# Optimization experiments

Measured on AMD Instinct MI355X. Metric: run time of the kernel, lower is better.

Reference implementation:

```python
import jax, jax.numpy as jnp
import numpy as np

D_MODEL = 256
N_HEADS = 8
HEAD_DIM = D_MODEL // N_HEADS  # 32
N_LEVELS = 4
N_POINTS = 4
LEVEL_SHAPES = [(100, 100), (50, 50), (25, 25), (13, 13)]
LEVEL_STARTS = [0] + list(np.cumsum([h * w for h, w in LEVEL_SHAPES]))[:-1]
LEN_IN = int(sum(h * w for h, w in LEVEL_SHAPES))  # 13294
BATCH = 2
LEN_Q = LEN_IN  # encoder self-attention


def _offset_bias():
    # faithful to MSDeformAttn._reset_parameters for sampling_offsets bias
    thetas = np.arange(N_HEADS, dtype=np.float32) * (2.0 * np.pi / N_HEADS)
    grid = np.stack([np.cos(thetas), np.sin(thetas)], -1)
    grid = grid / np.abs(grid).max(-1, keepdims=True)
    grid = np.tile(grid.reshape(N_HEADS, 1, 1, 2), (1, N_LEVELS, N_POINTS, 1))
    for i in range(N_POINTS):
        grid[:, :, i, :] *= i + 1
    return jnp.asarray(grid.reshape(-1), dtype=jnp.float32)


def setup_inputs() -> dict:
    key = jax.random.key(0)
    ks = jax.random.split(key, 10)
    s = 1.0 / np.sqrt(D_MODEL)
    inp = {
        "query": jax.random.normal(ks[0], (BATCH, LEN_Q, D_MODEL), jnp.float32),
        "reference_points": jax.random.uniform(ks[1], (BATCH, LEN_Q, N_LEVELS, 2), jnp.float32),
        "input_flatten": jax.random.normal(ks[2], (BATCH, LEN_IN, D_MODEL), jnp.float32),
        "input_spatial_shapes": jnp.asarray(LEVEL_SHAPES, dtype=jnp.int32),
        "W_value": jax.random.normal(ks[3], (D_MODEL, D_MODEL), jnp.float32) * s,
        "b_value": jnp.zeros((D_MODEL,), jnp.float32),
        "W_off": jax.random.normal(ks[4], (D_MODEL, N_HEADS * N_LEVELS * N_POINTS * 2), jnp.float32) * 0.01,
        "b_off": _offset_bias(),
        "W_attn": jax.random.normal(ks[5], (D_MODEL, N_HEADS * N_LEVELS * N_POINTS), jnp.float32) * 0.01,
        "b_attn": jnp.zeros((N_HEADS * N_LEVELS * N_POINTS,), jnp.float32),
        "W_out": jax.random.normal(ks[6], (D_MODEL, D_MODEL), jnp.float32) * s,
        "b_out": jnp.zeros((D_MODEL,), jnp.float32),
    }
    return inp


def _corner(v_t, ix, iy, h, w):
    # v_t: (n, M, h*w, D); ix/iy: (n, M, LqP) int32. Zero padding outside.
    valid = (ix >= 0) & (ix < w) & (iy >= 0) & (iy < h)
    idx = jnp.clip(iy, 0, h - 1) * w + jnp.clip(ix, 0, w - 1)
    g = jnp.take_along_axis(v_t, idx[..., None], axis=2)  # (n, M, LqP, D)
    return g * valid[..., None].astype(v_t.dtype)


def _ms_deform_attn(query, reference_points, input_flatten,
                    W_value, b_value, W_off, b_off, W_attn, b_attn, W_out, b_out):
    n, lq, _ = query.shape
    value = (input_flatten @ W_value + b_value).reshape(n, LEN_IN, N_HEADS, HEAD_DIM)
    offs = (query @ W_off + b_off).reshape(n, lq, N_HEADS, N_LEVELS, N_POINTS, 2)
    aw = jax.nn.softmax(
        (query @ W_attn + b_attn).reshape(n, lq, N_HEADS, N_LEVELS * N_POINTS), axis=-1
    ).reshape(n, lq, N_HEADS, N_LEVELS, N_POINTS)
    # offset_normalizer = (w, h) per level
    norm = jnp.asarray([[w, h] for h, w in LEVEL_SHAPES], dtype=query.dtype)
    loc = reference_points[:, :, None, :, None, :] + offs / norm[None, None, None, :, None, :]

    acc = jnp.zeros((n, N_HEADS, lq, HEAD_DIM), dtype=value.dtype)
    for l, (h, w) in enumerate(LEVEL_SHAPES):
        s0 = LEVEL_STARTS[l]
        v_t = jnp.transpose(value[:, s0:s0 + h * w], (0, 2, 1, 3))  # (n, M, hw, D)
        ll = loc[:, :, :, l]  # (n, lq, M, P, 2) in [0,1]
        # grid_sample bilinear, align_corners=False: pixel = coord*size - 0.5
        x = ll[..., 0] * w - 0.5
        y = ll[..., 1] * h - 0.5
        x0 = jnp.floor(x); y0 = jnp.floor(y)
        tx = x - x0; ty = y - y0
        ix0 = x0.astype(jnp.int32); iy0 = y0.astype(jnp.int32)
        flat = lambda a: jnp.transpose(a, (0, 2, 1, 3)).reshape(n, N_HEADS, lq * N_POINTS)
        ix0f, iy0f = flat(ix0), flat(iy0)
        txf = flat(tx)[..., None]; tyf = flat(ty)[..., None]
        g00 = _corner(v_t, ix0f, iy0f, h, w)
        g01 = _corner(v_t, ix0f + 1, iy0f, h, w)
        g10 = _corner(v_t, ix0f, iy0f + 1, h, w)
        g11 = _corner(v_t, ix0f + 1, iy0f + 1, h, w)
        samp = (g00 * (1 - txf) * (1 - tyf) + g01 * txf * (1 - tyf)
                + g10 * (1 - txf) * tyf + g11 * txf * tyf)
        samp = samp.reshape(n, N_HEADS, lq, N_POINTS, HEAD_DIM)
        wl = jnp.transpose(aw[:, :, :, l], (0, 2, 1, 3))[..., None]  # (n, M, lq, P, 1)
        acc = acc + (samp * wl).sum(axis=3)

    out = jnp.transpose(acc, (0, 2, 1, 3)).reshape(n, lq, D_MODEL)
    return out @ W_out + b_out


def reference(query, reference_points, input_flatten, input_spatial_shapes,
              W_value, b_value, W_off, b_off, W_attn, b_attn, W_out, b_out):
    # input_spatial_shapes carried for signature fidelity; level geometry is static.
    return _ms_deform_attn(query, reference_points, input_flatten,
                           W_value, b_value, W_off, b_off, W_attn, b_attn, W_out, b_out)
```

## Files before the change

### kernel.cpp

```cpp
#include <hip/hip_runtime.h>

#define NH 8
#define HD 32
#define NL 4
#define NP 4
#define DM 256
#define LEN_IN_C 13294
#define LQ_C 13294
#define B_C 2
#define M_TOTAL (B_C * LQ_C)
#define MT_TILES 1662
#define MT_PAD 1664
#define RBLK (MT_PAD / 4)

typedef __attribute__((ext_vector_type(8))) short short8;
typedef __attribute__((ext_vector_type(4))) float floatx4;

__device__ __forceinline__ unsigned short f2bf(float x) {
    union { float f; unsigned int u; } a; a.f = x;
    unsigned int r = (a.u + 0x7FFFu + ((a.u >> 16) & 1u)) >> 16;
    return (unsigned short)r;
}
__device__ __forceinline__ float bflo(unsigned int u) {
    union { unsigned int u; float f; } a; a.u = u << 16; return a.f;
}
__device__ __forceinline__ float bfhi(unsigned int u) {
    union { unsigned int u; float f; } a; a.u = u & 0xffff0000u; return a.f;
}

__device__ __forceinline__ void glds16(const void* g, void* l) {
    __builtin_amdgcn_global_load_lds(
        (const __attribute__((address_space(1))) unsigned int*)g,
        (__attribute__((address_space(3))) unsigned int*)l, 16, 0, 0);
}

__global__ __launch_bounds__(256) void conv_a_kernel(const float* __restrict__ A0,
                                                     unsigned short* __restrict__ D0,
                                                     const float* __restrict__ A1,
                                                     unsigned short* __restrict__ D1,
                                                     int M) {
    const float* A = blockIdx.y ? A1 : A0;
    unsigned short* Asw = blockIdx.y ? D1 : D0;
    const int u = blockIdx.x * 256 + threadIdx.x;
    const int lane = u & 63;
    const int kc = (u >> 6) & 7;
    const int rt = u >> 9;
    const int row = rt * 16 + (lane & 15);
    const int col0 = kc * 32 + (lane >> 4) * 8;
    unsigned short tmp[8];
    if (row < M) {
        const float4 f0 = *(const float4*)(A + (size_t)row * 256 + col0);
        const float4 f1 = *(const float4*)(A + (size_t)row * 256 + col0 + 4);
        tmp[0] = f2bf(f0.x); tmp[1] = f2bf(f0.y); tmp[2] = f2bf(f0.z); tmp[3] = f2bf(f0.w);
        tmp[4] = f2bf(f1.x); tmp[5] = f2bf(f1.y); tmp[6] = f2bf(f1.z); tmp[7] = f2bf(f1.w);
    } else {
#pragma unroll
        for (int j = 0; j < 8; ++j) tmp[j] = 0;
    }
    short8 v;
#pragma unroll
    for (int j = 0; j < 8; ++j) v[j] = (short)tmp[j];
    ((short8*)Asw)[u] = v;
}

__device__ __forceinline__ void conv_b_body(const float* __restrict__ W,
                                            unsigned short* __restrict__ Bsw,
                                            int Nsrc, int NTsrc, int NTtotal, int ntOff,
                                            int vblk) {
    const int u = vblk * 256 + threadIdx.x;
    const int lane = u & 63;
    const int unit = u >> 6;
    const int ntl = unit % NTsrc;
    const int kc = unit / NTsrc;
    const int n = ntl * 16 + (lane & 15);
    const int k0 = kc * 32 + (lane >> 4) * 8;
    short8 v;
#pragma unroll
    for (int j = 0; j < 8; ++j)
        v[j] = (short)f2bf(W[(size_t)(k0 + j) * Nsrc + n]);
    ((short8*)Bsw)[(size_t)(kc * NTtotal + ntOff + ntl) * 64 + lane] = v;
}

__global__ __launch_bounds__(256) void conv_weights_kernel(const float* __restrict__ Wv,
                                                           const float* __restrict__ Woff,
                                                           const float* __restrict__ Wattn,
                                                           const float* __restrict__ Wout,
                                                           const float* __restrict__ boff,
                                                           const float* __restrict__ battn,
                                                           unsigned short* __restrict__ BswV,
                                                           unsigned short* __restrict__ BswOA,
                                                           unsigned short* __restrict__ BswO,
                                                           float* __restrict__ fbias) {
    const int blk = blockIdx.x;
    if (blk < 32)        conv_b_body(Wv,    BswV,  256, 16, 16, 0,  blk);
    else if (blk < 64)   conv_b_body(Woff,  BswOA, 256, 16, 24, 0,  blk - 32);
    else if (blk < 80)   conv_b_body(Wattn, BswOA, 128,  8, 24, 16, blk - 64);
    else if (blk < 112)  conv_b_body(Wout,  BswO,  256, 16, 16, 0,  blk - 80);
    else {
        const int t = (blk - 112) * 256 + threadIdx.x;
        if (t < 384) fbias[t] = (t < 256) ? boff[t] : battn[t - 256];
    }
}

template <bool OUT_BF16, int NT_B, int NCOLS>
__device__ __forceinline__ void gemm_lds_body(short8* As, short8* Bs,
                                              const short8* __restrict__ Au,
                                              const short8* __restrict__ Bu,
                                              int rtile0, int ntB,
                                              const float* __restrict__ bias,
                                              void* __restrict__ Cout, int M) {
    const int tid = threadIdx.x;
    const int lane = tid & 63;
    const int wave = tid >> 6;

#pragma unroll
    for (int i = 0; i < 8; ++i)
        glds16(&Au[(size_t)((rtile0 + wave) * 8 + i) * 64 + lane], &As[(wave * 8 + i) * 64]);
#pragma unroll
    for (int j = 0; j < 2; ++j) {
        const int u = wave * 2 + j;
        glds16(&Bu[(size_t)(ntB + u) * 64 + lane], &Bs[u * 64]);
    }
    __syncthreads();

    floatx4 acc[4][2];
#pragma unroll
    for (int r = 0; r < 4; ++r)
#pragma unroll
        for (int j = 0; j < 2; ++j) acc[r][j] = (floatx4){0.f, 0.f, 0.f, 0.f};

#pragma unroll
    for (int kc = 0; kc < 8; ++kc) {
        if (kc < 7) {
#pragma unroll
            for (int j = 0; j < 2; ++j) {
                const int u = wave * 2 + j;
                glds16(&Bu[(size_t)((kc + 1) * NT_B + ntB + u) * 64 + lane],
                       &Bs[(((kc + 1) & 1) * 8 + u) * 64]);
            }
        }
        const short8 a0 = As[(0 * 8 + kc) * 64 + lane];
        const short8 a1 = As[(1 * 8 + kc) * 64 + lane];
        const short8 a2 = As[(2 * 8 + kc) * 64 + lane];
        const short8 a3 = As[(3 * 8 + kc) * 64 + lane];
        const short8 b0 = Bs[((kc & 1) * 8 + wave * 2 + 0) * 64 + lane];
        const short8 b1 = Bs[((kc & 1) * 8 + wave * 2 + 1) * 64 + lane];
        acc[0][0] = __builtin_amdgcn_mfma_f32_16x16x32_bf16(a0, b0, acc[0][0], 0, 0, 0);
        acc[0][1] = __builtin_amdgcn_mfma_f32_16x16x32_bf16(a0, b1, acc[0][1], 0, 0, 0);
        acc[1][0] = __builtin_amdgcn_mfma_f32_16x16x32_bf16(a1, b0, acc[1][0], 0, 0, 0);
        acc[1][1] = __builtin_amdgcn_mfma_f32_16x16x32_bf16(a1, b1, acc[1][1], 0, 0, 0);
        acc[2][0] = __builtin_amdgcn_mfma_f32_16x16x32_bf16(a2, b0, acc[2][0], 0, 0, 0);
        acc[2][1] = __builtin_amdgcn_mfma_f32_16x16x32_bf16(a2, b1, acc[2][1], 0, 0, 0);
        acc[3][0] = __builtin_amdgcn_mfma_f32_16x16x32_bf16(a3, b0, acc[3][0], 0, 0, 0);
        acc[3][1] = __builtin_amdgcn_mfma_f32_16x16x32_bf16(a3, b1, acc[3][1], 0, 0, 0);
        __syncthreads();
    }

    const int colq = lane & 15;
    const int rowq = (lane >> 4) * 4;
#pragma unroll
    for (int j = 0; j < 2; ++j) {
        const int col = (ntB + wave * 2 + j) * 16 + colq;
        const float bc = bias[col];
#pragma unroll
        for (int r = 0; r < 4; ++r) {
#pragma unroll
            for (int reg = 0; reg < 4; ++reg) {
                const int row = (rtile0 + r) * 16 + rowq + reg;
                if (row < M) {
                    const float v = acc[r][j][reg] + bc;
                    if (OUT_BF16)
                        ((unsigned short*)Cout)[(size_t)row * NCOLS + col] = f2bf(v);
                    else
                        ((float*)Cout)[(size_t)row * NCOLS + col] = v;
                }
            }
        }
    }
}

__global__ __launch_bounds__(256, 3) void dual_gemm_kernel(const short8* __restrict__ AuV,
                                                           const short8* __restrict__ AuQ,
                                                           const short8* __restrict__ BuV,
                                                           const short8* __restrict__ BuOA,
                                                           const float* __restrict__ bv,
                                                           const float* __restrict__ fbias,
                                                           unsigned short* __restrict__ value,
                                                           float* __restrict__ fused, int M) {
    __shared__ short8 As[32 * 64];
    __shared__ short8 Bs[16 * 64];
    const int rtile0 = blockIdx.x * 4;
    const int y = blockIdx.y;
    if (y < 2)
        gemm_lds_body<true, 16, 256>(As, Bs, AuV, BuV, rtile0, y * 8, bv, value, M);
    else
        gemm_lds_body<false, 24, 384>(As, Bs, AuQ, BuOA, rtile0, (y - 2) * 8, fbias, fused, M);
}

__global__ __launch_bounds__(256, 3) void out_gemm_kernel(const short8* __restrict__ AuAcc,
                                                          const short8* __restrict__ BuO,
                                                          const float* __restrict__ bout,
                                                          float* __restrict__ out, int M) {
    __shared__ short8 As[32 * 64];
    __shared__ short8 Bs[16 * 64];
    gemm_lds_body<false, 16, 256>(As, Bs, AuAcc, BuO, blockIdx.x * 4, blockIdx.y * 8,
                                  bout, out, M);
}

__global__ __launch_bounds__(256, 4) void msda_sample_kernel(const float* __restrict__ refp,
                                                             const unsigned short* __restrict__ value,
                                                             const float* __restrict__ fused,
                                                             unsigned short* __restrict__ AccSw) {
    constexpr int lvl_hw[4] = {100, 50, 25, 13};
    constexpr int lvl_s[4] = {0, 10000, 12500, 13125};

    const int bq0 = blockIdx.x * 4;
    const int tid = threadIdx.x;

    __shared__ float s_ref[32];
    __shared__ int4 s_pi[4 * 8 * 17];
    __shared__ float4 s_pw[4 * 8 * 17];

    if (tid < 32) s_ref[tid] = refp[(size_t)bq0 * 8 + tid];
    __syncthreads();

#pragma unroll
    for (int jj = 0; jj < 2; ++jj) {
        const int job = jj * 256 + tid;
        const int qq = job >> 7;
        const int t = job & 127;
        const int h = t >> 4;
        const int l = (t >> 2) & 3;
        const int bq = bq0 + qq;
        const int b = (bq >= LQ_C) ? 1 : 0;

        const float logit = fused[(size_t)bq * 384 + 256 + t];
        float mx = logit;
#pragma unroll
        for (int mask = 1; mask < 16; mask <<= 1) mx = fmaxf(mx, __shfl_xor(mx, mask));
        const float e = expf(logit - mx);
        float s = e;
#pragma unroll
        for (int mask = 1; mask < 16; mask <<= 1) s += __shfl_xor(s, mask);
        const float aw = e / s;

        const int whl = lvl_hw[l];
        const float fwh = (float)whl;
        const float2 oxy = *(const float2*)(fused + (size_t)bq * 384 + t * 2);
        const float x = s_ref[qq * 8 + l * 2] * fwh + oxy.x - 0.5f;
        const float y = s_ref[qq * 8 + l * 2 + 1] * fwh + oxy.y - 0.5f;
        const float x0f = floorf(x), y0f = floorf(y);
        const float tx = x - x0f, ty = y - y0f;
        const int ix0 = (int)x0f, iy0 = (int)y0f;

        const bool xv0 = (unsigned)ix0 < (unsigned)whl;
        const bool xv1 = (unsigned)(ix0 + 1) < (unsigned)whl;
        const bool yv0 = (unsigned)iy0 < (unsigned)whl;
        const bool yv1 = (unsigned)(iy0 + 1) < (unsigned)whl;

        const int cx0 = min(max(ix0, 0), whl - 1);
        const int cx1 = min(max(ix0 + 1, 0), whl - 1);
        const int cy0 = min(max(iy0, 0), whl - 1);
        const int cy1 = min(max(iy0 + 1, 0), whl - 1);

        const int base = (b * LEN_IN_C + lvl_s[l]) * 256 + h * 32;
        const int r0 = base + cy0 * (whl * 256);
        const int r1 = base + cy1 * (whl * 256);
        int4 ii;
        ii.x = (r0 + cx0 * 256) * 2;
        ii.y = (r0 + cx1 * 256) * 2;
        ii.z = (r1 + cx0 * 256) * 2;
        ii.w = (r1 + cx1 * 256) * 2;
        float4 wv;
        wv.x = (xv0 && yv0) ? aw * (1.f - tx) * (1.f - ty) : 0.f;
        wv.y = (xv1 && yv0) ? aw * tx * (1.f - ty) : 0.f;
        wv.z = (xv0 && yv1) ? aw * (1.f - tx) * ty : 0.f;
        wv.w = (xv1 && yv1) ? aw * tx * ty : 0.f;
        const int slot = (qq * 8 + h) * 17 + (t & 15);
        s_pi[slot] = ii;
        s_pw[slot] = wv;
    }
    __syncthreads();

    const int qq = tid >> 6;
    const int h = (tid >> 3) & 7;
    const int l8 = tid & 7;
    const char* vbp = (const char*)value + l8 * 8;
    const int pbase = (qq * 8 + h) * 17;

    float4 acc0 = {0.f, 0.f, 0.f, 0.f};
    float4 acc1 = {0.f, 0.f, 0.f, 0.f};
#pragma unroll
    for (int g = 0; g < 4; ++g) {
        int4 ii[4]; float4 ww[4]; uint2 v[16];
#pragma unroll
        for (int p = 0; p < 4; ++p) {
            ii[p] = s_pi[pbase + g * 4 + p];
            ww[p] = s_pw[pbase + g * 4 + p];
        }
#pragma unroll
        for (int p = 0; p < 4; ++p) {
            v[p * 4 + 0] = *(const uint2*)(vbp + ii[p].x);
            v[p * 4 + 1] = *(const uint2*)(vbp + ii[p].y);
            v[p * 4 + 2] = *(const uint2*)(vbp + ii[p].z);
            v[p * 4 + 3] = *(const uint2*)(vbp + ii[p].w);
        }
#pragma unroll
        for (int p = 0; p < 4; ++p) {
            const float4 wv = ww[p];
            const uint2 v00 = v[p * 4 + 0], v01 = v[p * 4 + 1];
            const uint2 v10 = v[p * 4 + 2], v11 = v[p * 4 + 3];
            acc0.x += wv.x * bflo(v00.x); acc0.y += wv.x * bfhi(v00.x);
            acc0.z += wv.x * bflo(v00.y); acc0.w += wv.x * bfhi(v00.y);
            acc1.x += wv.y * bflo(v01.x); acc1.y += wv.y * bfhi(v01.x);
            acc1.z += wv.y * bflo(v01.y); acc1.w += wv.y * bfhi(v01.y);
            acc0.x += wv.z * bflo(v10.x); acc0.y += wv.z * bfhi(v10.x);
            acc0.z += wv.z * bflo(v10.y); acc0.w += wv.z * bfhi(v10.y);
            acc1.x += wv.w * bflo(v11.x); acc1.y += wv.w * bfhi(v11.x);
            acc1.z += wv.w * bflo(v11.y); acc1.w += wv.w * bfhi(v11.y);
        }
    }
    const float4 acc = {acc0.x + acc1.x, acc0.y + acc1.y, acc0.z + acc1.z, acc0.w + acc1.w};

    const int bq = bq0 + qq;
    const int rt = bq >> 4, mm = bq & 15;
    const int col = h * 32 + l8 * 4;
    const int kc = col >> 5, q2 = (col >> 3) & 3, j = col & 7;
    unsigned int p0 = (unsigned int)f2bf(acc.x) | ((unsigned int)f2bf(acc.y) << 16);
    unsigned int p1 = (unsigned int)f2bf(acc.z) | ((unsigned int)f2bf(acc.w) << 16);
    uint2 pk; pk.x = p0; pk.y = p1;
    *(uint2*)(AccSw + ((size_t)((rt * 8 + kc) * 64 + (q2 * 16 + mm)) * 8 + j)) = pk;
}

extern "C" void kernel_launch(void* const* d_in, const int* in_sizes, int n_in,
                              void* d_out, int out_size, void* d_ws, size_t ws_size,
                              hipStream_t stream) {
    const float* query  = (const float*)d_in[0];
    const float* refp   = (const float*)d_in[1];
    const float* inflat = (const float*)d_in[2];
    const float* Wv    = (const float*)d_in[4];
    const float* bv    = (const float*)d_in[5];
    const float* Woff  = (const float*)d_in[6];
    const float* boff  = (const float*)d_in[7];
    const float* Wattn = (const float*)d_in[8];
    const float* battn = (const float*)d_in[9];
    const float* Wout  = (const float*)d_in[10];
    const float* bout  = (const float*)d_in[11];
    float* out = (float*)d_out;

    char* p = (char*)d_ws;
    const size_t aswBytes = (size_t)MT_PAD * 8 * 64 * 8 * sizeof(unsigned short);
    unsigned short* AswV = (unsigned short*)p;           p += aswBytes;
    unsigned short* AswQ = (unsigned short*)p;           p += aswBytes;
    unsigned short* BswV = (unsigned short*)p;           p += (size_t)8 * 16 * 64 * 8 * 2;
    unsigned short* BswOA = (unsigned short*)p;          p += (size_t)8 * 24 * 64 * 8 * 2;
    unsigned short* BswO = (unsigned short*)p;           p += (size_t)8 * 16 * 64 * 8 * 2;
    float* fbias = (float*)p;                            p += 384 * sizeof(float);
    unsigned short* value = (unsigned short*)p;          p += (size_t)M_TOTAL * 256 * 2;
    float* fused = (float*)p;                            p += (size_t)M_TOTAL * 384 * 4;
    unsigned short* AccSw = AswV;

    const int M = M_TOTAL;

    conv_weights_kernel<<<114, 256, 0, stream>>>(Wv, Woff, Wattn, Wout, boff, battn,
                                                 BswV, BswOA, BswO, fbias);
    conv_a_kernel<<<dim3(MT_PAD * 2, 2), 256, 0, stream>>>(inflat, AswV, query, AswQ, M);
    dual_gemm_kernel<<<dim3(RBLK, 5), 256, 0, stream>>>((const short8*)AswV, (const short8*)AswQ,
                                                        (const short8*)BswV, (const short8*)BswOA,
                                                        bv, fbias, value, fused, M);
    msda_sample_kernel<<<M / 4, 256, 0, stream>>>(refp, value, fused, AccSw);
    out_gemm_kernel<<<dim3(RBLK, 2), 256, 0, stream>>>((const short8*)AccSw, (const short8*)BswO,
                                                       bout, out, M);
}
```

Baseline: 231.1 us.

## Head-major value layout, row-pair sampling, 64-col GEMM tiles, merged conversion kernels

Merges the weight and activation bf16 conversion kernels into one launch. The GEMMs now use 64-column tiles with all of B preloaded into LDS, which removes the per-k syncthreads and double buffering, and the grid is reordered so column blocks vary fastest. The value projection is written head-major so each sampling row segment is contiguous. The sampler therefore loads two 16-byte row pairs per point, with x-clamped edge weights, instead of four 8-byte corners, then reduces across half-lanes with a shuffle. This trades more blocks and a lower occupancy bound for fewer, wider gathers and fewer barriers.

Result: slower. 298.4 us (+29.1%).

```diff
diff --git a/kernel.cpp b/kernel.cpp
--- a/kernel.cpp
+++ b/kernel.cpp
@@ -34,35 +34,6 @@
         (__attribute__((address_space(3))) unsigned int*)l, 16, 0, 0);
 }
 
-__global__ __launch_bounds__(256) void conv_a_kernel(const float* __restrict__ A0,
-                                                     unsigned short* __restrict__ D0,
-                                                     const float* __restrict__ A1,
-                                                     unsigned short* __restrict__ D1,
-                                                     int M) {
-    const float* A = blockIdx.y ? A1 : A0;
-    unsigned short* Asw = blockIdx.y ? D1 : D0;
-    const int u = blockIdx.x * 256 + threadIdx.x;
-    const int lane = u & 63;
-    const int kc = (u >> 6) & 7;
-    const int rt = u >> 9;
-    const int row = rt * 16 + (lane & 15);
-    const int col0 = kc * 32 + (lane >> 4) * 8;
-    unsigned short tmp[8];
-    if (row < M) {
-        const float4 f0 = *(const float4*)(A + (size_t)row * 256 + col0);
-        const float4 f1 = *(const float4*)(A + (size_t)row * 256 + col0 + 4);
-        tmp[0] = f2bf(f0.x); tmp[1] = f2bf(f0.y); tmp[2] = f2bf(f0.z); tmp[3] = f2bf(f0.w);
-        tmp[4] = f2bf(f1.x); tmp[5] = f2bf(f1.y); tmp[6] = f2bf(f1.z); tmp[7] = f2bf(f1.w);
-    } else {
-#pragma unroll
-        for (int j = 0; j < 8; ++j) tmp[j] = 0;
-    }
-    short8 v;
-#pragma unroll
-    for (int j = 0; j < 8; ++j) v[j] = (short)tmp[j];
-    ((short8*)Asw)[u] = v;
-}
-
 __device__ __forceinline__ void conv_b_body(const float* __restrict__ W,
                                             unsigned short* __restrict__ Bsw,
                                             int Nsrc, int NTsrc, int NTtotal, int ntOff,
@@ -81,105 +52,119 @@
     ((short8*)Bsw)[(size_t)(kc * NTtotal + ntOff + ntl) * 64 + lane] = v;
 }
 
-__global__ __launch_bounds__(256) void conv_weights_kernel(const float* __restrict__ Wv,
-                                                           const float* __restrict__ Woff,
-                                                           const float* __restrict__ Wattn,
-                                                           const float* __restrict__ Wout,
-                                                           const float* __restrict__ boff,
-                                                           const float* __restrict__ battn,
-                                                           unsigned short* __restrict__ BswV,
-                                                           unsigned short* __restrict__ BswOA,
-                                                           unsigned short* __restrict__ BswO,
-                                                           float* __restrict__ fbias) {
-    const int blk = blockIdx.x;
-    if (blk < 32)        conv_b_body(Wv,    BswV,  256, 16, 16, 0,  blk);
-    else if (blk < 64)   conv_b_body(Woff,  BswOA, 256, 16, 24, 0,  blk - 32);
-    else if (blk < 80)   conv_b_body(Wattn, BswOA, 128,  8, 24, 16, blk - 64);
-    else if (blk < 112)  conv_b_body(Wout,  BswO,  256, 16, 16, 0,  blk - 80);
-    else {
-        const int t = (blk - 112) * 256 + threadIdx.x;
-        if (t < 384) fbias[t] = (t < 256) ? boff[t] : battn[t - 256];
-    }
-}
-
-template <bool OUT_BF16, int NT_B, int NCOLS>
-__device__ __forceinline__ void gemm_lds_body(short8* As, short8* Bs,
-                                              const short8* __restrict__ Au,
-                                              const short8* __restrict__ Bu,
-                                              int rtile0, int ntB,
-                                              const float* __restrict__ bias,
-                                              void* __restrict__ Cout, int M) {
+__global__ __launch_bounds__(256) void conv_all_kernel(const float* __restrict__ A0,
+                                                       unsigned short* __restrict__ D0,
+                                                       const float* __restrict__ A1,
+                                                       unsigned short* __restrict__ D1,
+                                                       const float* __restrict__ Wv,
+                                                       const float* __restrict__ Woff,
+                                                       const float* __restrict__ Wattn,
+                                                       const float* __restrict__ Wout,
+                                                       const float* __restrict__ boff,
+                                                       const float* __restrict__ battn,
+                                                       unsigned short* __restrict__ BswV,
+                                                       unsigned short* __restrict__ BswOA,
+                                                       unsigned short* __restrict__ BswO,
+                                                       float* __restrict__ fbias,
+                                                       int M) {
+    const int bx = blockIdx.x;
+    if (bx < MT_PAD * 2) {
+        const float* A = blockIdx.y ? A1 : A0;
+        unsigned short* Asw = blockIdx.y ? D1 : D0;
+        const int u = bx * 256 + threadIdx.x;
+        const int lane = u & 63;
+        const int kc = (u >> 6) & 7;
+        const int rt = u >> 9;
+        const int row = rt * 16 + (lane & 15);
+        const int col0 = kc * 32 + (lane >> 4) * 8;
+        unsigned short tmp[8];
+        if (row < M) {
+            const float4 f0 = *(const float4*)(A + (size_t)row * 256 + col0);
+            const float4 f1 = *(const float4*)(A + (size_t)row * 256 + col0 + 4);
+            tmp[0] = f2bf(f0.x); tmp[1] = f2bf(f0.y); tmp[2] = f2bf(f0.z); tmp[3] = f2bf(f0.w);
+            tmp[4] = f2bf(f1.x); tmp[5] = f2bf(f1.y); tmp[6] = f2bf(f1.z); tmp[7] = f2bf(f1.w);
+        } else {
+#pragma unroll
+            for (int j = 0; j < 8; ++j) tmp[j] = 0;
+        }
+        short8 v;
+#pragma unroll
+        for (int j = 0; j < 8; ++j) v[j] = (short)tmp[j];
+        ((short8*)Asw)[u] = v;
+    } else {
+        const int wblk = (bx - MT_PAD * 2) + 57 * blockIdx.y;
+        if (wblk < 32)       conv_b_body(Wv,    BswV,  256, 16, 16, 0,  wblk);
+        else if (wblk < 64)  conv_b_body(Woff,  BswOA, 256, 16, 24, 0,  wblk - 32);
+        else if (wblk < 80)  conv_b_body(Wattn, BswOA, 128,  8, 24, 16, wblk - 64);
+        else if (wblk < 112) conv_b_body(Wout,  BswO,  256, 16, 16, 0,  wblk - 80);
+        else {
+            const int t = threadIdx.x;
+            if (t < 384) fbias[t] = (t < 256) ? boff[t] : battn[t - 256];
+        }
+    }
+}
+
+template <bool VAL_LAYOUT, int NT_B, int NCOLS>
+__device__ __forceinline__ void gemm64_body(short8* As, short8* Bs,
+                                            const short8* __restrict__ Au,
+                                            const short8* __restrict__ Bu,
+                                            int rtile0, int ntB,
+                                            const float* __restrict__ bias,
+                                            void* __restrict__ Cout, int M) {
     const int tid = threadIdx.x;
     const int lane = tid & 63;
     const int wave = tid >> 6;
 
 #pragma unroll
-    for (int i = 0; i < 8; ++i)
-        glds16(&Au[(size_t)((rtile0 + wave) * 8 + i) * 64 + lane], &As[(wave * 8 + i) * 64]);
-#pragma unroll
-    for (int j = 0; j < 2; ++j) {
-        const int u = wave * 2 + j;
-        glds16(&Bu[(size_t)(ntB + u) * 64 + lane], &Bs[u * 64]);
+    for (int i = 0; i < 16; ++i) {
+        const int u = wave * 16 + i;
+        if (u < 32) {
+            glds16(&Au[(size_t)((rtile0 + (u >> 3)) * 8 + (u & 7)) * 64 + lane], &As[u * 64]);
+        } else {
+            const int v = u - 32;
+            glds16(&Bu[(size_t)((v >> 2) * NT_B + ntB + (v & 3)) * 64 + lane], &Bs[v * 64]);
+        }
     }
     __syncthreads();
 
-    floatx4 acc[4][2];
-#pragma unroll
-    for (int r = 0; r < 4; ++r)
-#pragma unroll
-        for (int j = 0; j < 2; ++j) acc[r][j] = (floatx4){0.f, 0.f, 0.f, 0.f};
+    floatx4 acc[4];
+#pragma unroll
+    for (int r = 0; r < 4; ++r) acc[r] = (floatx4){0.f, 0.f, 0.f, 0.f};
 
 #pragma unroll
     for (int kc = 0; kc < 8; ++kc) {
-        if (kc < 7) {
-#pragma unroll
-            for (int j = 0; j < 2; ++j) {
-                const int u = wave * 2 + j;
-                glds16(&Bu[(size_t)((kc + 1) * NT_B + ntB + u) * 64 + lane],
-                       &Bs[(((kc + 1) & 1) * 8 + u) * 64]);
-            }
-        }
+        const short8 b  = Bs[(kc * 4 + wave) * 64 + lane];
         const short8 a0 = As[(0 * 8 + kc) * 64 + lane];
         const short8 a1 = As[(1 * 8 + kc) * 64 + lane];
         const short8 a2 = As[(2 * 8 + kc) * 64 + lane];
         const short8 a3 = As[(3 * 8 + kc) * 64 + lane];
-        const short8 b0 = Bs[((kc & 1) * 8 + wave * 2 + 0) * 64 + lane];
-        const short8 b1 = Bs[((kc & 1) * 8 + wave * 2 + 1) * 64 + lane];
-        acc[0][0] = __builtin_amdgcn_mfma_f32_16x16x32_bf16(a0, b0, acc[0][0], 0, 0, 0);
-        acc[0][1] = __builtin_amdgcn_mfma_f32_16x16x32_bf16(a0, b1, acc[0][1], 0, 0, 0);
-        acc[1][0] = __builtin_amdgcn_mfma_f32_16x16x32_bf16(a1, b0, acc[1][0], 0, 0, 0);
-        acc[1][1] = __builtin_amdgcn_mfma_f32_16x16x32_bf16(a1, b1, acc[1][1], 0, 0, 0);
-        acc[2][0] = __builtin_amdgcn_mfma_f32_16x16x32_bf16(a2, b0, acc[2][0], 0, 0, 0);
-        acc[2][1] = __builtin_amdgcn_mfma_f32_16x16x32_bf16(a2, b1, acc[2][1], 0, 0, 0);
-        acc[3][0] = __builtin_amdgcn_mfma_f32_16x16x32_bf16(a3, b0, acc[3][0], 0, 0, 0);
-        acc[3][1] = __builtin_amdgcn_mfma_f32_16x16x32_bf16(a3, b1, acc[3][1], 0, 0, 0);
-        __syncthreads();
+        acc[0] = __builtin_amdgcn_mfma_f32_16x16x32_bf16(a0, b, acc[0], 0, 0, 0);
+        acc[1] = __builtin_amdgcn_mfma_f32_16x16x32_bf16(a1, b, acc[1], 0, 0, 0);
+        acc[2] = __builtin_amdgcn_mfma_f32_16x16x32_bf16(a2, b, acc[2], 0, 0, 0);
+        acc[3] = __builtin_amdgcn_mfma_f32_16x16x32_bf16(a3, b, acc[3], 0, 0, 0);
     }
 
     const int colq = lane & 15;
     const int rowq = (lane >> 4) * 4;
-#pragma unroll
-    for (int j = 0; j < 2; ++j) {
-        const int col = (ntB + wave * 2 + j) * 16 + colq;
-        const float bc = bias[col];
-#pragma unroll
-        for (int r = 0; r < 4; ++r) {
-#pragma unroll
-            for (int reg = 0; reg < 4; ++reg) {
-                const int row = (rtile0 + r) * 16 + rowq + reg;
-                if (row < M) {
-                    const float v = acc[r][j][reg] + bc;
-                    if (OUT_BF16)
-                        ((unsigned short*)Cout)[(size_t)row * NCOLS + col] = f2bf(v);
-                    else
-                        ((float*)Cout)[(size_t)row * NCOLS + col] = v;
-                }
+    const int col = (ntB + wave) * 16 + colq;
+    const float bc = bias[col];
+#pragma unroll
+    for (int r = 0; r < 4; ++r) {
+#pragma unroll
+        for (int reg = 0; reg < 4; ++reg) {
+            const int row = (rtile0 + r) * 16 + rowq + reg;
+            if (row < M) {
+                const float v = acc[r][reg] + bc;
+                if (VAL_LAYOUT)
+                    ((unsigned short*)Cout)[((size_t)(col >> 5) * M + row) * 32 + (col & 31)] = f2bf(v);
+                else
+                    ((float*)Cout)[(size_t)row * NCOLS + col] = v;
             }
         }
     }
 }
 
-__global__ __launch_bounds__(256, 3) void dual_gemm_kernel(const short8* __restrict__ AuV,
+__global__ __launch_bounds__(256, 2) void dual_gemm_kernel(const short8* __restrict__ AuV,
                                                            const short8* __restrict__ AuQ,
                                                            const short8* __restrict__ BuV,
                                                            const short8* __restrict__ BuOA,
@@ -188,23 +173,23 @@
                                                            unsigned short* __restrict__ value,
                                                            float* __restrict__ fused, int M) {
     __shared__ short8 As[32 * 64];
-    __shared__ short8 Bs[16 * 64];
-    const int rtile0 = blockIdx.x * 4;
-    const int y = blockIdx.y;
-    if (y < 2)
-        gemm_lds_body<true, 16, 256>(As, Bs, AuV, BuV, rtile0, y * 8, bv, value, M);
+    __shared__ short8 Bs[32 * 64];
+    const int rtile0 = blockIdx.y * 4;
+    const int x = blockIdx.x;
+    if (x < 4)
+        gemm64_body<true, 16, 256>(As, Bs, AuV, BuV, rtile0, x * 4, bv, value, M);
     else
-        gemm_lds_body<false, 24, 384>(As, Bs, AuQ, BuOA, rtile0, (y - 2) * 8, fbias, fused, M);
-}
-
-__global__ __launch_bounds__(256, 3) void out_gemm_kernel(const short8* __restrict__ AuAcc,
+        gemm64_body<false, 24, 384>(As, Bs, AuQ, BuOA, rtile0, (x - 4) * 4, fbias, fused, M);
+}
+
+__global__ __launch_bounds__(256, 2) void out_gemm_kernel(const short8* __restrict__ AuAcc,
                                                           const short8* __restrict__ BuO,
                                                           const float* __restrict__ bout,
                                                           float* __restrict__ out, int M) {
     __shared__ short8 As[32 * 64];
-    __shared__ short8 Bs[16 * 64];
-    gemm_lds_body<false, 16, 256>(As, Bs, AuAcc, BuO, blockIdx.x * 4, blockIdx.y * 8,
-                                  bout, out, M);
+    __shared__ short8 Bs[32 * 64];
+    gemm64_body<false, 16, 256>(As, Bs, AuAcc, BuO, blockIdx.y * 4, blockIdx.x * 4,
+                                bout, out, M);
 }
 
 __global__ __launch_bounds__(256, 4) void msda_sample_kernel(const float* __restrict__ refp,
@@ -218,7 +203,7 @@
     const int tid = threadIdx.x;
 
     __shared__ float s_ref[32];
-    __shared__ int4 s_pi[4 * 8 * 17];
+    __shared__ int2 s_pi[4 * 8 * 17];
     __shared__ float4 s_pw[4 * 8 * 17];
 
     if (tid < 32) s_ref[tid] = refp[(size_t)bq0 * 8 + tid];
@@ -253,31 +238,29 @@
         const float tx = x - x0f, ty = y - y0f;
         const int ix0 = (int)x0f, iy0 = (int)y0f;
 
-        const bool xv0 = (unsigned)ix0 < (unsigned)whl;
-        const bool xv1 = (unsigned)(ix0 + 1) < (unsigned)whl;
         const bool yv0 = (unsigned)iy0 < (unsigned)whl;
         const bool yv1 = (unsigned)(iy0 + 1) < (unsigned)whl;
-
-        const int cx0 = min(max(ix0, 0), whl - 1);
-        const int cx1 = min(max(ix0 + 1, 0), whl - 1);
         const int cy0 = min(max(iy0, 0), whl - 1);
         const int cy1 = min(max(iy0 + 1, 0), whl - 1);
 
-        const int base = (b * LEN_IN_C + lvl_s[l]) * 256 + h * 32;
-        const int r0 = base + cy0 * (whl * 256);
-        const int r1 = base + cy1 * (whl * 256);
-        int4 ii;
-        ii.x = (r0 + cx0 * 256) * 2;
-        ii.y = (r0 + cx1 * 256) * 2;
-        ii.z = (r1 + cx0 * 256) * 2;
-        ii.w = (r1 + cx1 * 256) * 2;
+        const int bxc = min(max(ix0, 0), whl - 2);
+        const float wx0 = 1.f - tx, wx1 = tx;
+        const float c0w = (ix0 == bxc) ? wx0 : ((ix0 + 1 == bxc) ? wx1 : 0.f);
+        const float c1w = (ix0 == bxc) ? wx1 : ((ix0 == bxc + 1) ? wx0 : 0.f);
+
+        const int base = (h * M_TOTAL + b * LEN_IN_C + lvl_s[l]) * 32;
+        int2 off;
+        off.x = (base + (cy0 * whl + bxc) * 32) * 2;
+        off.y = (base + (cy1 * whl + bxc) * 32) * 2;
+        const float a0 = aw * (1.f - ty) * (yv0 ? 1.f : 0.f);
+        const float a1 = aw * ty * (yv1 ? 1.f : 0.f);
         float4 wv;
-        wv.x = (xv0 && yv0) ? aw * (1.f - tx) * (1.f - ty) : 0.f;
-        wv.y = (xv1 && yv0) ? aw * tx * (1.f - ty) : 0.f;
-        wv.z = (xv0 && yv1) ? aw * (1.f - tx) * ty : 0.f;
-        wv.w = (xv1 && yv1) ? aw * tx * ty : 0.f;
+        wv.x = a0 * c0w;
+        wv.y = a0 * c1w;
+        wv.z = a1 * c0w;
+        wv.w = a1 * c1w;
         const int slot = (qq * 8 + h) * 17 + (t & 15);
-        s_pi[slot] = ii;
+        s_pi[slot] = off;
         s_pw[slot] = wv;
     }
     __syncthreads();
@@ -285,51 +268,51 @@
     const int qq = tid >> 6;
     const int h = (tid >> 3) & 7;
     const int l8 = tid & 7;
-    const char* vbp = (const char*)value + l8 * 8;
+    const int half = l8 >> 2;
+    const char* vbp = (const char*)value + l8 * 16;
     const int pbase = (qq * 8 + h) * 17;
 
-    float4 acc0 = {0.f, 0.f, 0.f, 0.f};
-    float4 acc1 = {0.f, 0.f, 0.f, 0.f};
+    float acc[8] = {0.f, 0.f, 0.f, 0.f, 0.f, 0.f, 0.f, 0.f};
 #pragma unroll
     for (int g = 0; g < 4; ++g) {
-        int4 ii[4]; float4 ww[4]; uint2 v[16];
+        int2 off[4]; float4 ww[4]; uint4 r0[4], r1[4];
 #pragma unroll
         for (int p = 0; p < 4; ++p) {
-            ii[p] = s_pi[pbase + g * 4 + p];
+            off[p] = s_pi[pbase + g * 4 + p];
             ww[p] = s_pw[pbase + g * 4 + p];
         }
 #pragma unroll
         for (int p = 0; p < 4; ++p) {
-            v[p * 4 + 0] = *(const uint2*)(vbp + ii[p].x);
-            v[p * 4 + 1] = *(const uint2*)(vbp + ii[p].y);
-            v[p * 4 + 2] = *(const uint2*)(vbp + ii[p].z);
-            v[p * 4 + 3] = *(const uint2*)(vbp + ii[p].w);
+            r0[p] = *(const uint4*)(vbp + off[p].x);
+            r1[p] = *(const uint4*)(vbp + off[p].y);
         }
 #pragma unroll
         for (int p = 0; p < 4; ++p) {
-            const float4 wv = ww[p];
-            const uint2 v00 = v[p * 4 + 0], v01 = v[p * 4 + 1];
-            const uint2 v10 = v[p * 4 + 2], v11 = v[p * 4 + 3];
-            acc0.x += wv.x * bflo(v00.x); acc0.y += wv.x * bfhi(v00.x);
-            acc0.z += wv.x * bflo(v00.y); acc0.w += wv.x * bfhi(v00.y);
-            acc1.x += wv.y * bflo(v01.x); acc1.y += wv.y * bfhi(v01.x);
-            acc1.z += wv.y * bflo(v01.y); acc1.w += wv.y * bfhi(v01.y);
-            acc0.x += wv.z * bflo(v10.x); acc0.y += wv.z * bfhi(v10.x);
-            acc0.z += wv.z * bflo(v10.y); acc0.w += wv.z * bfhi(v10.y);
-            acc1.x += wv.w * bflo(v11.x); acc1.y += wv.w * bfhi(v11.x);
-            acc1.z += wv.w * bflo(v11.y); acc1.w += wv.w * bfhi(v11.y);
-        }
-    }
-    const float4 acc = {acc0.x + acc1.x, acc0.y + acc1.y, acc0.z + acc1.z, acc0.w + acc1.w};
-
-    const int bq = bq0 + qq;
-    const int rt = bq >> 4, mm = bq & 15;
-    const int col = h * 32 + l8 * 4;
-    const int kc = col >> 5, q2 = (col >> 3) & 3, j = col & 7;
-    unsigned int p0 = (unsigned int)f2bf(acc.x) | ((unsigned int)f2bf(acc.y) << 16);
-    unsigned int p1 = (unsigned int)f2bf(acc.z) | ((unsigned int)f2bf(acc.w) << 16);
-    uint2 pk; pk.x = p0; pk.y = p1;
-    *(uint2*)(AccSw + ((size_t)((rt * 8 + kc) * 64 + (q2 * 16 + mm)) * 8 + j)) = pk;
+            const float w0 = half ? ww[p].y : ww[p].x;
+            const float w1 = half ? ww[p].w : ww[p].z;
+            acc[0] += w0 * bflo(r0[p].x); acc[1] += w0 * bfhi(r0[p].x);
+            acc[2] += w0 * bflo(r0[p].y); acc[3] += w0 * bfhi(r0[p].y);
+            acc[4] += w0 * bflo(r0[p].z); acc[5] += w0 * bfhi(r0[p].z);
+            acc[6] += w0 * bflo(r0[p].w); acc[7] += w0 * bfhi(r0[p].w);
+            acc[0] += w1 * bflo(r1[p].x); acc[1] += w1 * bfhi(r1[p].x);
+            acc[2] += w1 * bflo(r1[p].y); acc[3] += w1 * bfhi(r1[p].y);
+            acc[4] += w1 * bflo(r1[p].z); acc[5] += w1 * bfhi(r1[p].z);
+            acc[6] += w1 * bflo(r1[p].w); acc[7] += w1 * bfhi(r1[p].w);
+        }
+    }
+#pragma unroll
+    for (int i = 0; i < 8; ++i) acc[i] += __shfl_xor(acc[i], 4);
+
+    if (half == 0) {
+        const int bq = bq0 + qq;
+        const int rt = bq >> 4, mm = bq & 15;
+        uint4 pk;
+        pk.x = (unsigned)f2bf(acc[0]) | ((unsigned)f2bf(acc[1]) << 16);
+        pk.y = (unsigned)f2bf(acc[2]) | ((unsigned)f2bf(acc[3]) << 16);
+        pk.z = (unsigned)f2bf(acc[4]) | ((unsigned)f2bf(acc[5]) << 16);
+        pk.w = (unsigned)f2bf(acc[6]) | ((unsigned)f2bf(acc[7]) << 16);
+        *(uint4*)(AccSw + (size_t)((rt * 8 + h) * 64 + (l8 * 16 + mm)) * 8) = pk;
+    }
 }
 
 extern "C" void kernel_launch(void* const* d_in, const int* in_sizes, int n_in,
@@ -362,13 +345,14 @@
 
     const int M = M_TOTAL;
 
-    conv_weights_kernel<<<114, 256, 0, stream>>>(Wv, Woff, Wattn, Wout, boff, battn,
-                                                 BswV, BswOA, BswO, fbias);
-    conv_a_kernel<<<dim3(MT_PAD * 2, 2), 256, 0, stream>>>(inflat, AswV, query, AswQ, M);
-    dual_gemm_kernel<<<dim3(RBLK, 5), 256, 0, stream>>>((const short8*)AswV, (const short8*)AswQ,
-                                                        (const short8*)BswV, (const short8*)BswOA,
-                                                        bv, fbias, value, fused, M);
+    conv_all_kernel<<<dim3(MT_PAD * 2 + 57, 2), 256, 0, stream>>>(
+        inflat, AswV, query, AswQ, Wv, Woff, Wattn, Wout, boff, battn,
+        BswV, BswOA, BswO, fbias, M);
+    dual_gemm_kernel<<<dim3(10, RBLK), 256, 0, stream>>>(
+        (const short8*)AswV, (const short8*)AswQ,
+        (const short8*)BswV, (const short8*)BswOA,
+        bv, fbias, value, fused, M);
     msda_sample_kernel<<<M / 4, 256, 0, stream>>>(refp, value, fused, AccSw);
-    out_gemm_kernel<<<dim3(RBLK, 2), 256, 0, stream>>>((const short8*)AccSw, (const short8*)BswO,
-                                                       bout, out, M);
-}
+    out_gemm_kernel<<<dim3(4, RBLK), 256, 0, stream>>>(
+        (const short8*)AccSw, (const short8*)BswO, bout, out, M);
+}
```
